# Performance work log

Measured on AMD Instinct MI355X. Metric: run time of the kernel, lower is better.

The kernel has to match this reference:

```python
import jax, jax.numpy as jnp
import numpy as np

DM = 1024; NHEAD = 16; HD = 64; ROPE = 32; KVC = 256; QC = 384
NSEQ = 4; SPS = 256; S = NSEQ * SPS + 1; B = 2
SCALE = 1.0 / ((HD + ROPE) // 2)          # 1/48, per module
LAMBDA_INIT = 0.8 - 0.6 * float(np.exp(-0.3 * 0))  # depth=0 -> 0.2
EPS_RMS = 1.1920929e-07                   # torch default RMSNorm eps (finfo eps)
EPS_HEAD = 1e-5


def _make_freqs(sps):
    # precompute_freqs_cis with args.seq_len=SPS, qk_rope_dim=ROPE (YaRN correction)
    dim = ROPE // 2
    base = 10000.0
    factor = 40.0
    seq_len = SPS
    max_seqlen = seq_len * 4
    freqs = 1.0 / base ** (np.arange(0, dim, 2, dtype=np.float32) / dim)  # (dim//2,)

    def corr_dim(nr):
        return dim * np.log(seq_len / (nr * 2 * np.pi)) / (2 * np.log(base))

    low = max(int(np.floor(corr_dim(32.0))), 0)
    high = min(int(np.ceil(corr_dim(1.0))), dim - 1)
    if low == high:
        high = high + 0.001
    ramp = np.clip((np.arange(dim // 2, dtype=np.float32) - low) / (high - low), 0, 1)
    smooth = 1.0 - ramp
    freqs = freqs / factor * (1 - smooth) + freqs * smooth
    t = np.arange(max_seqlen, dtype=np.float32)
    ang = np.outer(t, freqs)  # (max_seqlen, dim//2)
    return np.cos(ang)[:sps].astype(np.float32), np.sin(ang)[:sps].astype(np.float32)


def _make_mask():
    # global-separator mask: column 0 attendable, rest = tiled causal-per-timestep blocks
    temp = np.triu(np.ones((SPS, SPS), dtype=np.int32), k=1)
    tiled = np.tile(temp, (NSEQ, NSEQ))
    full = np.ones((S, S), dtype=np.int32)
    full[:, 0] = 0
    full[1:, 1:] = tiled
    return full[None, None]  # (1,1,S,S), 1 = masked


def _rms(x, g, eps):
    return x * jax.lax.rsqrt(jnp.mean(x * x, axis=-1, keepdims=True) + eps) * g


def _rope(x, cos, sin):
    # x: (b, nseq, sps, 2*nhead, ROPE//2) -> rotate complex pairs in last dim
    b, ns, sps, h, d = x.shape
    xr = x.reshape(b, ns, sps, h, d // 2, 2)
    c = cos[None, None, :, None, :]
    s = sin[None, None, :, None, :]
    yr = xr[..., 0] * c - xr[..., 1] * s
    yi = xr[..., 0] * s + xr[..., 1] * c
    return jnp.stack([yr, yi], axis=-1).reshape(b, ns, sps, h, d)


def setup_inputs() -> dict:
    key = jax.random.key(0)
    ks = jax.random.split(key, 12)
    cos, sin = _make_freqs(SPS)
    inp = {
        "x": jax.random.normal(ks[0], (B, S, DM), dtype=jnp.float32),
        "mask": jnp.asarray(_make_mask()),
        "freqs_cos": jnp.asarray(cos),
        "freqs_sin": jnp.asarray(sin),
        "W_kv_down": jax.random.normal(ks[1], (DM, KVC + ROPE), dtype=jnp.float32) * 0.02,
        "W_q_down": jax.random.normal(ks[2], (DM, QC), dtype=jnp.float32) * 0.02,
        "W_kv_up": jax.random.normal(ks[3], (KVC, NHEAD * HD * 2), dtype=jnp.float32) * 0.02,
        "W_q_up": jax.random.normal(ks[4], (QC, NHEAD * (HD + ROPE)), dtype=jnp.float32) * 0.02,
        "W_o": jax.random.normal(ks[5], (NHEAD * HD, DM), dtype=jnp.float32) * 0.02,
        "g_kv_norm": jnp.ones((KVC,), dtype=jnp.float32),
        "g_q_norm": jnp.ones((QC,), dtype=jnp.float32),
        "g_head_norm": jnp.ones((HD,), dtype=jnp.float32),
        "lambda_q1": jax.random.normal(ks[6], (HD // 2,), dtype=jnp.float32) * 0.1,
        "lambda_k1": jax.random.normal(ks[7], (HD // 2,), dtype=jnp.float32) * 0.1,
        "lambda_q2": jax.random.normal(ks[8], (HD // 2,), dtype=jnp.float32) * 0.1,
        "lambda_k2": jax.random.normal(ks[9], (HD // 2,), dtype=jnp.float32) * 0.1,
    }
    return inp


def reference(x, mask, freqs_cos, freqs_sin, W_kv_down, W_q_down, W_kv_up, W_q_up,
              W_o, g_kv_norm, g_q_norm, g_head_norm,
              lambda_q1, lambda_k1, lambda_q2, lambda_k2):
    b, s, _ = x.shape
    sps = (s - 1) // NSEQ
    # KV latent compression
    ckv = x @ W_kv_down                                   # (b,S,KVC+ROPE)
    c_kv, k_rope = ckv[..., :KVC], ckv[..., KVC:]
    kv = _rms(c_kv, g_kv_norm, EPS_RMS) @ W_kv_up         # (b,S,NHEAD*2*HD)
    kv = kv.reshape(b, s, NHEAD, 2 * HD)
    k, v = kv[..., :HD], kv[..., HD:]
    k = k.reshape(b, s, NHEAD * 2, HD // 2)               # dual head-groups
    # Q latent compression
    qf = _rms(x @ W_q_down, g_q_norm, EPS_RMS) @ W_q_up
    qf = qf.reshape(b, s, NHEAD, HD + ROPE)
    q, q_rope = qf[..., :HD], qf[..., HD:]
    q = q.reshape(b, s, NHEAD * 2, HD // 2)
    # RoPE parts: shared k_rope tiled over heads, then split into dual groups
    k_rope = jnp.tile(k_rope[:, :, None, :], (1, 1, NHEAD, 1)).reshape(b, s, NHEAD * 2, ROPE // 2)
    q_rope = q_rope.reshape(b, s, NHEAD * 2, ROPE // 2)
    # rotate all positions except the global separator token (index 0)
    q_rot = _rope(q_rope[:, 1:].reshape(b, NSEQ, sps, NHEAD * 2, ROPE // 2), freqs_cos, freqs_sin)
    k_rot = _rope(k_rope[:, 1:].reshape(b, NSEQ, sps, NHEAD * 2, ROPE // 2), freqs_cos, freqs_sin)
    q_rope = jnp.concatenate([q_rope[:, :1], q_rot.reshape(b, s - 1, NHEAD * 2, ROPE // 2)], axis=1)
    k_rope = jnp.concatenate([k_rope[:, :1], k_rot.reshape(b, s - 1, NHEAD * 2, ROPE // 2)], axis=1)
    q = jnp.concatenate([q, q_rope], axis=-1).transpose(0, 2, 1, 3)  # (b,2H,S,48)
    k = jnp.concatenate([k, k_rope], axis=-1).transpose(0, 2, 1, 3)
    v = v.transpose(0, 2, 1, 3)                                      # (b,H,S,64)
    # cognitive (signed) softmax attention
    a = jnp.einsum('bhqd,bhkd->bhqk', q, k) * SCALE
    abs_a = jnp.where(mask == 1, -1e9, jnp.abs(a))
    a = jnp.sign(a) * jax.nn.softmax(abs_a, axis=-1)
    # differential combination of dual head-groups
    lam = (jnp.exp(jnp.sum(lambda_q1 * lambda_k1)) -
           jnp.exp(jnp.sum(lambda_q2 * lambda_k2)) + LAMBDA_INIT)
    a = a.reshape(b, NHEAD, 2, s, s)
    G = jnp.mean(a[:, :, 0], axis=-1, keepdims=True)
    a = a[:, :, 0] - lam * a[:, :, 1] + G * lam
    a = jnp.where(mask == 1, 0.0, a)
    out = jnp.einsum('bhqk,bhkd->bhqd', a, v).transpose(0, 2, 1, 3)  # (b,S,H,64)
    out = _rms(out, g_head_norm, EPS_HEAD)
    return out.reshape(b, s, NHEAD * HD) @ W_o
```

## Files before the change

### kernel.cpp

```cpp
#include <hip/hip_runtime.h>
#include <hip/hip_bf16.h>
#include <math.h>

#define NHEAD 16
#define SEQ 1025
#define BATCH 2
#define NH2 32
#define KSCALE (1.0f/48.0f)
#define EPS_RMS 1.1920929e-07f
#define EPS_HEAD 1e-05f
#define LAMBDA_INIT 0.2f
#define R_TOT (BATCH*SEQ)

typedef __attribute__((ext_vector_type(8))) short bf16x8;
typedef __attribute__((ext_vector_type(4))) float f32x4;
typedef __attribute__((ext_vector_type(4))) int  i32x4;

static __device__ __forceinline__ unsigned short f2bf(float x) {
    unsigned int u = __float_as_uint(x);
    unsigned int r = (u + 0x7fffu + ((u >> 16) & 1u)) >> 16;
    return (unsigned short)r;
}
static __device__ __forceinline__ float bf2f(unsigned short h) {
    return __uint_as_float(((unsigned int)h) << 16);
}
static __device__ __forceinline__ void split3(float v, unsigned short& h,
                                              unsigned short& m, unsigned short& l) {
    h = f2bf(v); float r1 = v - bf2f(h);
    m = f2bf(r1); float r2 = r1 - bf2f(m);
    l = f2bf(r2);
}
static __device__ __forceinline__ f32x4 MFMA(bf16x8 a, bf16x8 b, f32x4 c) {
    return __builtin_amdgcn_mfma_f32_16x16x32_bf16(a, b, c, 0, 0, 0);
}

__global__ __launch_bounds__(256) void conv_all(
    const float* __restrict__ x, const float* __restrict__ Wkvd,
    const float* __restrict__ Wqd, const float* __restrict__ Wkvu,
    const float* __restrict__ Wqu, const float* __restrict__ Wo,
    unsigned short* __restrict__ xh, unsigned short* __restrict__ xm,
    unsigned short* __restrict__ xl,
    unsigned short* __restrict__ Wdh, unsigned short* __restrict__ Wdm,
    unsigned short* __restrict__ Wdl,
    unsigned short* __restrict__ Wuh, unsigned short* __restrict__ Wum,
    unsigned short* __restrict__ Wul,
    unsigned short* __restrict__ Wqh, unsigned short* __restrict__ Wqm,
    unsigned short* __restrict__ Wql,
    unsigned short* __restrict__ Wo1)
{
    __shared__ float tile[32][33];
    int bid = blockIdx.x, tid = threadIdx.x;
    if (bid < 2050) {
        int i = bid * 1024 + tid * 4;
        f32x4 v = *(const f32x4*)(x + i);
#pragma unroll
        for (int j = 0; j < 4; ++j) {
            unsigned short h, m, l;
            split3(v[j], h, m, l);
            xh[i + j] = h; xm[i + j] = m; xl[i + j] = l;
        }
        return;
    }
    bid -= 2050;
    const float* W; unsigned short *Th, *Tm, *Tl; int K, N, gx;
    if (bid < 288)              { W = Wkvd; Th = Wdh; Tm = Wdm; Tl = Wdl; K = 1024; N = 288;  gx = 9;  }
    else if ((bid -= 288) < 384){ W = Wqd;  Th = Wdh + (size_t)288*1024; Tm = Wdm + (size_t)288*1024;
                                  Tl = Wdl + (size_t)288*1024; K = 1024; N = 384; gx = 12; }
    else if ((bid -= 384) < 512){ W = Wkvu; Th = Wuh; Tm = Wum; Tl = Wul; K = 256;  N = 2048; gx = 64; }
    else if ((bid -= 512) < 576){ W = Wqu;  Th = Wqh; Tm = Wqm; Tl = Wql; K = 384;  N = 1536; gx = 48; }
    else { bid -= 576;            W = Wo;   Th = Wo1; Tm = nullptr; Tl = nullptr; K = 1024; N = 1024; gx = 32; }

    int n0 = (bid % gx) * 32, k0 = (bid / gx) * 32;
    int tx = tid & 31, ty = tid >> 5;
    for (int kk = ty; kk < 32; kk += 8)
        tile[kk][tx] = W[(size_t)(k0 + kk) * N + n0 + tx];
    __syncthreads();
    for (int nn = ty; nn < 32; nn += 8) {
        int n = n0 + nn, k = k0 + tx;
        float v = tile[tx][nn];
        if (Tm) {
            unsigned short h, m, l;
            split3(v, h, m, l);
            Th[(size_t)n * K + k] = h;
            Tm[(size_t)n * K + k] = m;
            Tl[(size_t)n * K + k] = l;
        } else {
            Th[(size_t)n * K + k] = f2bf(v);
        }
    }
}

__device__ __forceinline__ void gemm3_body(
    unsigned short* LA, unsigned short* LB,
    const unsigned short* __restrict__ Ah, const unsigned short* __restrict__ Am,
    const unsigned short* __restrict__ Al,
    const unsigned short* __restrict__ Bh, const unsigned short* __restrict__ Bm,
    const unsigned short* __restrict__ Bl,
    float* __restrict__ C,
    unsigned short* __restrict__ D0, unsigned short* __restrict__ D1,
    unsigned short* __restrict__ D2, unsigned short* __restrict__ D3,
    const float* __restrict__ fcos, const float* __restrict__ fsin,
    int M, int N, int K, int kb, int ke, int epi, int bm, int bn)
{
    int tid = threadIdx.x;
    int wid = tid >> 6, lane = tid & 63;
    int la = lane & 15, lb = lane >> 4;
    int wr = (wid >> 1) * 64, wc = (wid & 1) * 64;
    int wr4 = wr >> 4, wc4 = wc >> 4;

    const unsigned short* APl[3] = {Ah, Am, Al};
    const unsigned short* BPl[3] = {Bh, Bm, Bl};

    f32x4 acc[4][4];
#pragma unroll
    for (int m = 0; m < 4; ++m)
#pragma unroll
        for (int n = 0; n < 4; ++n) acc[m][n] = (f32x4){0.f, 0.f, 0.f, 0.f};

    auto LDF = [&](bf16x8* dst, const unsigned short* Lb, int p, int rb) {
#pragma unroll
        for (int q = 0; q < 4; ++q)
            dst[q] = *(const bf16x8*)&Lb[p * 4096 + ((rb + q) * 64 + lane) * 8];
    };
    auto MM = [&](bf16x8* av, bf16x8* bv) {
#pragma unroll
        for (int m = 0; m < 4; ++m)
#pragma unroll
            for (int n = 0; n < 4; ++n)
                acc[m][n] = MFMA(av[m], bv[n], acc[m][n]);
    };

    for (int k0 = kb; k0 < ke; k0 += 32) {
        __syncthreads();
#pragma unroll
        for (int p = 0; p < 3; ++p) {
#pragma unroll
            for (int it = 0; it < 2; ++it) {
                int k2 = tid + it * 256;
                int g = k2 >> 6, pos = k2 & 63;
                int row = (g << 4) + (pos & 15);
                int kc = (pos >> 4) * 8;
                i32x4 v = {0, 0, 0, 0}, w = {0, 0, 0, 0};
                int gr = bm + row;
                if (gr < M) v = *(const i32x4*)(APl[p] + (size_t)gr * K + k0 + kc);
                *(i32x4*)&LA[p * 4096 + k2 * 8] = v;
                int gn = bn + row;
                if (gn < N) w = *(const i32x4*)(BPl[p] + (size_t)gn * K + k0 + kc);
                *(i32x4*)&LB[p * 4096 + k2 * 8] = w;
            }
        }
        __syncthreads();
        bf16x8 av[4], bv0[4], bv1[4], bvt[4];
        LDF(av, LA, 0, wr4); LDF(bv0, LB, 0, wc4);
        LDF(bv1, LB, 1, wc4); LDF(bvt, LB, 2, wc4);
        __builtin_amdgcn_s_setprio(1);
        MM(av, bv0); MM(av, bv1); MM(av, bvt);
        __builtin_amdgcn_s_setprio(0);
        LDF(bvt, LA, 1, wr4);
        __builtin_amdgcn_s_setprio(1);
        MM(bvt, bv0); MM(bvt, bv1);
        __builtin_amdgcn_s_setprio(0);
        LDF(bvt, LA, 2, wr4);
        __builtin_amdgcn_s_setprio(1);
        MM(bvt, bv0);
        __builtin_amdgcn_s_setprio(0);
    }

#pragma unroll
    for (int m = 0; m < 4; ++m)
#pragma unroll
        for (int n = 0; n < 4; ++n) {
            int gc = bn + wc + n * 16 + la;
#pragma unroll
            for (int r = 0; r < 4; ++r) {
                int gr = bm + wr + m * 16 + lb * 4 + r;
                float v = acc[m][n][r];
                if (epi == 0) {
                    if (gr < M && gc < N) C[(size_t)gr * N + gc] = v;
                } else if (epi == 1) {
                    if (gr < M) {
                        int b = gr / SEQ, s = gr - b * SEQ;
                        int h2 = gc >> 7, rem = gc & 127;
                        if (rem < 64) {
                            int H = 2 * h2 + (rem >> 5), d = rem & 31;
                            size_t idx = (((size_t)b * NH2 + H) * SEQ + s) * 48 + d;
                            unsigned short hh, mm2, ll;
                            split3(v, hh, mm2, ll);
                            D0[idx] = hh; D1[idx] = mm2; D2[idx] = ll;
                        } else {
                            D3[(((size_t)b * NHEAD + h2) * SEQ + s) * 64 + (rem - 64)] = f2bf(v);
                        }
                    }
                } else {
                    float pv = __shfl_xor(v, 1);
                    if (gr < M) {
                        int b = gr / SEQ, s = gr - b * SEQ;
                        int h2 = gc / 96, rem = gc - h2 * 96;
                        int H, d; float outv;
                        if (rem < 64) {
                            H = 2 * h2 + (rem >> 5); d = rem & 31; outv = v;
                        } else {
                            int dd = rem - 64;
                            int e = dd >> 4, j = (dd & 15) >> 1;
                            H = 2 * h2 + e; d = 32 + (dd & 15);
                            if (s != 0) {
                                int p = (s - 1) & 255;
                                float cc = fcos[p * 8 + j], sn = fsin[p * 8 + j];
                                outv = ((la & 1) == 0) ? (v * cc - pv * sn)
                                                       : (pv * sn + v * cc);
                            } else outv = v;
                        }
                        outv *= KSCALE;
                        size_t idx = (((size_t)b * NH2 + H) * SEQ + s) * 48 + d;
                        unsigned short hh, mm2, ll;
                        split3(outv, hh, mm2, ll);
                        D0[idx] = hh; D1[idx] = mm2; D2[idx] = ll;
                    }
                }
            }
        }
}

__global__ __launch_bounds__(256) void gemm_down(
    const unsigned short* __restrict__ Ah, const unsigned short* __restrict__ Am,
    const unsigned short* __restrict__ Al,
    const unsigned short* __restrict__ Bh, const unsigned short* __restrict__ Bm,
    const unsigned short* __restrict__ Bl,
    float* __restrict__ C0, float* __restrict__ C1)
{
    __shared__ __align__(16) unsigned short LA[3 * 4096];
    __shared__ __align__(16) unsigned short LB[3 * 4096];
    int z = blockIdx.z;
    gemm3_body(LA, LB, Ah, Am, Al, Bh, Bm, Bl, z ? C1 : C0,
               nullptr, nullptr, nullptr, nullptr, nullptr, nullptr,
               R_TOT, 672, 1024, z * 512, z * 512 + 512, 0,
               blockIdx.y * 128, blockIdx.x * 128);
}

__global__ __launch_bounds__(256) void gemm_up(
    const unsigned short* __restrict__ cnh, const unsigned short* __restrict__ cnm,
    const unsigned short* __restrict__ cnl,
    const unsigned short* __restrict__ Wuh, const unsigned short* __restrict__ Wum,
    const unsigned short* __restrict__ Wul,
    const unsigned short* __restrict__ qnh, const unsigned short* __restrict__ qnm,
    const unsigned short* __restrict__ qnl,
    const unsigned short* __restrict__ Wqh, const unsigned short* __restrict__ Wqm,
    const unsigned short* __restrict__ Wql,
    unsigned short* __restrict__ Kah, unsigned short* __restrict__ Kam,
    unsigned short* __restrict__ Kal, unsigned short* __restrict__ Va,
    unsigned short* __restrict__ Qah, unsigned short* __restrict__ Qam,
    unsigned short* __restrict__ Qal,
    const float* __restrict__ fcos, const float* __restrict__ fsin)
{
    __shared__ __align__(16) unsigned short LA[3 * 4096];
    __shared__ __align__(16) unsigned short LB[3 * 4096];
    bool isq = (blockIdx.x >= 16);
    if (!isq)
        gemm3_body(LA, LB, cnh, cnm, cnl, Wuh, Wum, Wul, nullptr,
                   Kah, Kam, Kal, Va, nullptr, nullptr,
                   R_TOT, 2048, 256, 0, 256, 1, blockIdx.y * 128, blockIdx.x * 128);
    else
        gemm3_body(LA, LB, qnh, qnm, qnl, Wqh, Wqm, Wql, nullptr,
                   Qah, Qam, Qal, nullptr, fcos, fsin,
                   R_TOT, 1536, 384, 0, 384, 2, blockIdx.y * 128, (blockIdx.x - 16) * 128);
}

__global__ __launch_bounds__(256) void gemm_out(
    const unsigned short* __restrict__ Ah, const unsigned short* __restrict__ Bh,
    float* __restrict__ C, int M, int N, int K)
{
    __shared__ __align__(16) unsigned short As[4096];
    __shared__ __align__(16) unsigned short Bs[4096];
    int tid = threadIdx.x;
    int wid = tid >> 6, lane = tid & 63;
    int la = lane & 15, lb = lane >> 4;
    int bm = blockIdx.y * 128, bn = blockIdx.x * 128;
    int wr = (wid >> 1) * 64, wc = (wid & 1) * 64;
    int wr4 = wr >> 4, wc4 = wc >> 4;
    f32x4 acc[4][4];
#pragma unroll
    for (int m = 0; m < 4; ++m)
#pragma unroll
        for (int n = 0; n < 4; ++n) acc[m][n] = (f32x4){0.f, 0.f, 0.f, 0.f};
    for (int k0 = 0; k0 < K; k0 += 32) {
        __syncthreads();
#pragma unroll
        for (int it = 0; it < 2; ++it) {
            int k2 = tid + it * 256;
            int g = k2 >> 6, pos = k2 & 63;
            int row = (g << 4) + (pos & 15);
            int kc = (pos >> 4) * 8;
            i32x4 v = {0, 0, 0, 0}, w = {0, 0, 0, 0};
            int gr = bm + row;
            if (gr < M) v = *(const i32x4*)(Ah + (size_t)gr * K + k0 + kc);
            *(i32x4*)&As[k2 * 8] = v;
            int gn = bn + row;
            if (gn < N) w = *(const i32x4*)(Bh + (size_t)gn * K + k0 + kc);
            *(i32x4*)&Bs[k2 * 8] = w;
        }
        __syncthreads();
        bf16x8 a_[4], b_[4];
#pragma unroll
        for (int m = 0; m < 4; ++m) a_[m] = *(const bf16x8*)&As[((wr4 + m) * 64 + lane) * 8];
#pragma unroll
        for (int n = 0; n < 4; ++n) b_[n] = *(const bf16x8*)&Bs[((wc4 + n) * 64 + lane) * 8];
        __builtin_amdgcn_s_setprio(1);
#pragma unroll
        for (int m = 0; m < 4; ++m)
#pragma unroll
            for (int n = 0; n < 4; ++n) acc[m][n] = MFMA(a_[m], b_[n], acc[m][n]);
        __builtin_amdgcn_s_setprio(0);
    }
#pragma unroll
    for (int m = 0; m < 4; ++m)
#pragma unroll
        for (int n = 0; n < 4; ++n) {
            int gc = bn + wc + n * 16 + la;
            if (gc >= N) continue;
#pragma unroll
            for (int r = 0; r < 4; ++r) {
                int gr = bm + wr + m * 16 + lb * 4 + r;
                if (gr < M) C[(size_t)gr * N + gc] = acc[m][n][r];
            }
        }
}

__global__ __launch_bounds__(256) void k_rmsrope3(
    const float* __restrict__ ckvqd, const float* __restrict__ ckvqd2,
    unsigned short* __restrict__ cnh, unsigned short* __restrict__ cnm,
    unsigned short* __restrict__ cnl,
    unsigned short* __restrict__ qnh, unsigned short* __restrict__ qnm,
    unsigned short* __restrict__ qnl,
    unsigned short* __restrict__ Kah, unsigned short* __restrict__ Kam,
    unsigned short* __restrict__ Kal,
    const float* __restrict__ gkv, const float* __restrict__ gq,
    const float* __restrict__ fcos, const float* __restrict__ fsin)
{
    __shared__ float red[256];
    __shared__ float rot[32];
    int row = blockIdx.x, tid = threadIdx.x;
    int b = row / SEQ, s = row - b * SEQ;
    const float* cp  = ckvqd  + (size_t)row * 672;
    const float* cp2 = ckvqd2 + (size_t)row * 672;
    float c0 = cp[tid] + cp2[tid];
    float q0 = cp[288 + tid] + cp2[288 + tid];
    float q1 = (tid < 128) ? (cp[544 + tid] + cp2[544 + tid]) : 0.f;

    red[tid] = c0 * c0;
    __syncthreads();
    for (int o = 128; o; o >>= 1) { if (tid < o) red[tid] += red[tid + o]; __syncthreads(); }
    float inv1 = rsqrtf(red[0] * (1.f / 256.f) + EPS_RMS);
    __syncthreads();
    red[tid] = q0 * q0 + q1 * q1;
    __syncthreads();
    for (int o = 128; o; o >>= 1) { if (tid < o) red[tid] += red[tid + o]; __syncthreads(); }
    float inv2 = rsqrtf(red[0] * (1.f / 384.f) + EPS_RMS);

    unsigned short h, m, l;
    split3(c0 * inv1 * gkv[tid], h, m, l);
    size_t ci = (size_t)row * 256 + tid;
    cnh[ci] = h; cnm[ci] = m; cnl[ci] = l;

    split3(q0 * inv2 * gq[tid], h, m, l);
    size_t qi = (size_t)row * 384 + tid;
    qnh[qi] = h; qnm[qi] = m; qnl[qi] = l;
    if (tid < 128) {
        split3(q1 * inv2 * gq[256 + tid], h, m, l);
        qnh[qi + 256] = h; qnm[qi + 256] = m; qnl[qi + 256] = l;
    }

    if (tid < 16) {
        float r0 = cp[256 + 2 * tid] + cp2[256 + 2 * tid];
        float r1 = cp[256 + 2 * tid + 1] + cp2[256 + 2 * tid + 1];
        float o0, o1;
        if (s == 0) { o0 = r0; o1 = r1; }
        else {
            int p = (s - 1) & 255;
            int j = tid & 7;
            float cc = fcos[p * 8 + j], sn = fsin[p * 8 + j];
            o0 = r0 * cc - r1 * sn;
            o1 = r0 * sn + r1 * cc;
        }
        rot[2 * tid] = o0; rot[2 * tid + 1] = o1;
    }
    __syncthreads();
    for (int t = tid; t < 512; t += 256) {
        int H = t >> 4, dd = t & 15;
        int e = H & 1;
        split3(rot[e * 16 + dd], h, m, l);
        size_t idx = (((size_t)b * NH2 + H) * SEQ + s) * 48 + 32 + dd;
        Kah[idx] = h; Kam[idx] = m; Kal[idx] = l;
    }
}

__global__ __launch_bounds__(256, 2) void k_attn8(
    const unsigned short* __restrict__ Qah, const unsigned short* __restrict__ Qam,
    const unsigned short* __restrict__ Qal,
    const unsigned short* __restrict__ Kah, const unsigned short* __restrict__ Kam,
    const unsigned short* __restrict__ Kal,
    const unsigned short* __restrict__ Va, const float* __restrict__ ghead,
    const float* __restrict__ lq1, const float* __restrict__ lk1,
    const float* __restrict__ lq2, const float* __restrict__ lk2,
    unsigned short* __restrict__ attO)
{
    __shared__ __align__(16) unsigned short KS[6][3072];
    __shared__ __align__(16) unsigned short Vt[4096];
    __shared__ __align__(16) unsigned short Pl[4][1024];

    int bid0 = blockIdx.x;
    int bid = (bid0 & 7) * 68 + (bid0 >> 3);
    int rt = bid % 17;
    int bh = bid / 17;
    int h = bh & 15, b = bh >> 4;
    int tid = threadIdx.x, wid = tid >> 6, lane = tid & 63;
    int la = lane & 15, lb = lane >> 4;
    int r0 = rt * 64, r0w = r0 + wid * 16;

    float e1 = 0.f, e2 = 0.f;
    for (int i = 0; i < 32; ++i) { e1 = fmaf(lq1[i], lk1[i], e1); e2 = fmaf(lq2[i], lk2[i], e2); }
    float lam = __expf(e1) - __expf(e2) + LAMBDA_INIT;

    int pr[4];
#pragma unroll
    for (int g = 0; g < 4; ++g) {
        int r = r0w + lb * 4 + g;
        pr[g] = (r >= 1 && r < SEQ) ? ((r - 1) & 255) : -1;
    }
    int rA = r0w + la;
    int prA = (rA >= 1 && rA < SEQ) ? ((rA - 1) & 255) : -1;

    int prm = -1;
    for (int i = 0; i < 64; ++i) {
        int r = r0 + i;
        if (r >= 1 && r < SEQ) { int p = (r - 1) & 255; prm = p > prm ? p : prm; }
    }

    const size_t hb1 = ((size_t)(b * NH2 + 2 * h)) * SEQ * 48;
    const size_t hb2 = ((size_t)(b * NH2 + 2 * h + 1)) * SEQ * 48;
    const unsigned short* vp = Va + ((size_t)(b * NHEAD + h)) * SEQ * 64;
    const unsigned short* KP[6] = {Kah + hb1, Kam + hb1, Kal + hb1,
                                   Kah + hb2, Kam + hb2, Kal + hb2};

    int qrow = r0w + la; if (qrow > SEQ - 1) qrow = SEQ - 1;
    bf16x8 zf;
#pragma unroll
    for (int u = 0; u < 8; ++u) zf[u] = 0;
    bf16x8 q1[3][2], q2[3][2];
    {
        const unsigned short* QPl[3] = {Qah, Qam, Qal};
#pragma unroll
        for (int p = 0; p < 3; ++p)
#pragma unroll
            for (int f = 0; f < 2; ++f) {
                if (f == 0 || lb < 2) {
                    q1[p][f] = *(const bf16x8*)(QPl[p] + hb1 + (size_t)qrow * 48 + 32 * f + lb * 8);
                    q2[p][f] = *(const bf16x8*)(QPl[p] + hb2 + (size_t)qrow * 48 + 32 * f + lb * 8);
                } else { q1[p][f] = zf; q2[p][f] = zf; }
            }
    }

    int colA, uA, colB = 0, uB = 0;
    {
        int ci = tid;
        colA = ((ci >> 6) << 4) + (ci & 15);
        uA = (ci >> 4) & 3;
        if (tid < 128) {
            int c2 = tid;
            colB = ((c2 >> 5) << 4) + (c2 & 15);
            uB = 4 + ((c2 >> 4) & 1);
        }
    }
    int cv0 = tid >> 3, uv0 = tid & 7;
    int cv1 = (tid + 256) >> 3, uv1 = tid & 7;

    i32x4 preA[6], preB[6], vv[2];
    auto LOADT = [&](int c0n) {
        int gcA = c0n + colA; if (gcA > SEQ - 1) gcA = SEQ - 1;
#pragma unroll
        for (int p = 0; p < 6; ++p)
            preA[p] = *(const i32x4*)(KP[p] + (size_t)gcA * 48 + uA * 8);
        if (tid < 128) {
            int gcB = c0n + colB; if (gcB > SEQ - 1) gcB = SEQ - 1;
#pragma unroll
            for (int p = 0; p < 6; ++p)
                preB[p] = *(const i32x4*)(KP[p] + (size_t)gcB * 48 + uB * 8);
        }
        int gv0 = c0n + cv0; if (gv0 > SEQ - 1) gv0 = SEQ - 1;
        vv[0] = *(const i32x4*)(vp + (size_t)gv0 * 64 + uv0 * 8);
        int gv1 = c0n + cv1; if (gv1 > SEQ - 1) gv1 = SEQ - 1;
        vv[1] = *(const i32x4*)(vp + (size_t)gv1 * 64 + uv1 * 8);
    };
    auto WRITET = [&]() {
#pragma unroll
        for (int p = 0; p < 6; ++p)
            *(i32x4*)&KS[p][tid * 8] = preA[p];
        if (tid < 128) {
#pragma unroll
            for (int p = 0; p < 6; ++p)
                *(i32x4*)&KS[p][2048 + tid * 8] = preB[p];
        }
#pragma unroll
        for (int it = 0; it < 2; ++it) {
            int cv = it ? cv1 : cv0, uv = it ? uv1 : uv0;
            unsigned short tmp[8];
            *(i32x4*)tmp = vv[it];
#pragma unroll
            for (int j = 0; j < 8; ++j) {
                int d = uv * 8 + j;
                int g = ((d >> 4) << 1) + (cv >> 5);
                int pos = (((cv & 31) >> 3) << 4) + (d & 15);
                Vt[g * 512 + pos * 8 + (cv & 7)] = tmp[j];
            }
        }
    };

    f32x4 O1[4], O2[4], VS[4];
#pragma unroll
    for (int nd = 0; nd < 4; ++nd) {
        O1[nd] = (f32x4){0.f, 0.f, 0.f, 0.f};
        O2[nd] = (f32x4){0.f, 0.f, 0.f, 0.f};
        VS[nd] = (f32x4){0.f, 0.f, 0.f, 0.f};
    }
    float dA1[4] = {0.f, 0.f, 0.f, 0.f}, dA2[4] = {0.f, 0.f, 0.f, 0.f};
    float gsA[4] = {0.f, 0.f, 0.f, 0.f};
    f32x4 z = (f32x4){0.f, 0.f, 0.f, 0.f};

    LOADT(0);
    WRITET();
    __syncthreads();

    for (int j = 0; j <= 16; ++j) {
        bool need = (j == 16) ? (prm >= 255)
                              : (((j & 3) == 0) || (prm >= 64 * (j & 3) - 1));
        if (!need) continue;
        int c0 = j * 64;

        int nj = -1;
        for (int t2 = j + 1; t2 <= 16; ++t2) {
            bool nd2 = (t2 == 16) ? (prm >= 255)
                                  : (((t2 & 3) == 0) || (prm >= 64 * (t2 & 3) - 1));
            if (nd2) { nj = t2; break; }
        }
        if (nj >= 0) LOADT(nj * 64);

        f32x4 s1[4], s2[4];
        __builtin_amdgcn_s_setprio(1);
#pragma unroll
        for (int n = 0; n < 4; ++n) {
            int g0 = n * 512 + lane * 8;
            int g1 = 2048 + n * 256 + (lane & 31) * 8;
            bf16x8 kh0 = *(const bf16x8*)&KS[0][g0];
            bf16x8 kh1 = *(const bf16x8*)&KS[0][g1];
            bf16x8 km0 = *(const bf16x8*)&KS[1][g0];
            bf16x8 km1 = *(const bf16x8*)&KS[1][g1];
            bf16x8 kl0 = *(const bf16x8*)&KS[2][g0];
            bf16x8 kl1 = *(const bf16x8*)&KS[2][g1];
            f32x4 s = z;
            s = MFMA(q1[0][0], kh0, s); s = MFMA(q1[0][1], kh1, s);
            s = MFMA(q1[0][0], km0, s); s = MFMA(q1[0][1], km1, s);
            s = MFMA(q1[1][0], kh0, s); s = MFMA(q1[1][1], kh1, s);
            s = MFMA(q1[0][0], kl0, s); s = MFMA(q1[0][1], kl1, s);
            s = MFMA(q1[1][0], km0, s); s = MFMA(q1[1][1], km1, s);
            s = MFMA(q1[2][0], kh0, s); s = MFMA(q1[2][1], kh1, s);
            s1[n] = s;
        }
#pragma unroll
        for (int n = 0; n < 4; ++n) {
            int g0 = n * 512 + lane * 8;
            int g1 = 2048 + n * 256 + (lane & 31) * 8;
            bf16x8 kh0 = *(const bf16x8*)&KS[3][g0];
            bf16x8 kh1 = *(const bf16x8*)&KS[3][g1];
            bf16x8 km0 = *(const bf16x8*)&KS[4][g0];
            bf16x8 km1 = *(const bf16x8*)&KS[4][g1];
            bf16x8 kl0 = *(const bf16x8*)&KS[5][g0];
            bf16x8 kl1 = *(const bf16x8*)&KS[5][g1];
            f32x4 s = z;
            s = MFMA(q2[0][0], kh0, s); s = MFMA(q2[0][1], kh1, s);
            s = MFMA(q2[0][0], km0, s); s = MFMA(q2[0][1], km1, s);
            s = MFMA(q2[1][0], kh0, s); s = MFMA(q2[1][1], kh1, s);
            s = MFMA(q2[0][0], kl0, s); s = MFMA(q2[0][1], kl1, s);
            s = MFMA(q2[1][0], km0, s); s = MFMA(q2[1][1], km1, s);
            s = MFMA(q2[2][0], kh0, s); s = MFMA(q2[2][1], kh1, s);
            s2[n] = s;
        }
        __builtin_amdgcn_s_setprio(0);

        unsigned short p1v[4][4], p2v[4][4];
#pragma unroll
        for (int n = 0; n < 4; ++n) {
            int c = c0 + n * 16 + la;
            bool cz = (c == 0);
            int cm = (c - 1) & 255;
            bool cin = (c < SEQ);
#pragma unroll
            for (int g = 0; g < 4; ++g) {
                bool al = cz || (cin && cm <= pr[g]);
                float a = s1[n][g];
                float sa = __builtin_copysignf(__expf(fabsf(a)), a);
                sa = al ? sa : 0.f;
                p1v[n][g] = (unsigned short)((__float_as_uint(sa) + 0x8000u) >> 16);
                gsA[g] += sa;
                dA1[g] += fabsf(sa);
                float bb = s2[n][g];
                float sb = __builtin_copysignf(__expf(fabsf(bb)), bb);
                sb = al ? sb : 0.f;
                p2v[n][g] = (unsigned short)((__float_as_uint(sb) + 0x8000u) >> 16);
                dA2[g] += fabsf(sb);
            }
        }

#pragma unroll
        for (int n = 0; n < 4; ++n) {
            int pb = (n >> 1) * 512 + (((n & 1) << 1) + (la >> 3)) * 128 + (la & 7);
#pragma unroll
            for (int g = 0; g < 4; ++g)
                Pl[wid][pb + (lb * 4 + g) * 8] = p1v[n][g];
        }
        __asm__ volatile("s_waitcnt lgkmcnt(0)" ::: "memory");
        __builtin_amdgcn_sched_barrier(0);
        bf16x8 p1a0 = *(const bf16x8*)&Pl[wid][lane * 8];
        bf16x8 p1a1 = *(const bf16x8*)&Pl[wid][512 + lane * 8];
#pragma unroll
        for (int n = 0; n < 4; ++n) {
            int pb = (n >> 1) * 512 + (((n & 1) << 1) + (la >> 3)) * 128 + (la & 7);
#pragma unroll
            for (int g = 0; g < 4; ++g)
                Pl[wid][pb + (lb * 4 + g) * 8] = p2v[n][g];
        }
        __asm__ volatile("s_waitcnt lgkmcnt(0)" ::: "memory");
        __builtin_amdgcn_sched_barrier(0);
        bf16x8 p2a0 = *(const bf16x8*)&Pl[wid][lane * 8];
        bf16x8 p2a1 = *(const bf16x8*)&Pl[wid][512 + lane * 8];

        bf16x8 p0[2];
#pragma unroll
        for (int f = 0; f < 2; ++f)
#pragma unroll
            for (int jb = 0; jb < 8; ++jb) {
                int c = c0 + 32 * f + lb * 8 + jb;
                bool al = (c == 0) || (c < SEQ && ((c - 1) & 255) <= prA);
                p0[f][jb] = al ? (short)0x3F80 : (short)0;
            }

        __builtin_amdgcn_s_setprio(1);
#pragma unroll
        for (int nd = 0; nd < 4; ++nd) {
            bf16x8 vb0 = *(const bf16x8*)&Vt[(nd * 2) * 512 + lane * 8];
            bf16x8 vb1 = *(const bf16x8*)&Vt[(nd * 2 + 1) * 512 + lane * 8];
            O1[nd] = MFMA(p1a0, vb0, O1[nd]);
            O1[nd] = MFMA(p1a1, vb1, O1[nd]);
            O2[nd] = MFMA(p2a0, vb0, O2[nd]);
            O2[nd] = MFMA(p2a1, vb1, O2[nd]);
            VS[nd] = MFMA(p0[0], vb0, VS[nd]);
            VS[nd] = MFMA(p0[1], vb1, VS[nd]);
        }
        __builtin_amdgcn_s_setprio(0);

        if (nj >= 0) {
            __syncthreads();
            WRITET();
            __syncthreads();
        }
    }

#pragma unroll
    for (int off = 1; off < 16; off <<= 1) {
#pragma unroll
        for (int g = 0; g < 4; ++g) {
            dA1[g] += __shfl_xor(dA1[g], off);
            dA2[g] += __shfl_xor(dA2[g], off);
            gsA[g] += __shfl_xor(gsA[g], off);
        }
    }

    float i1[4], i2g[4], Gl[4];
#pragma unroll
    for (int g = 0; g < 4; ++g) {
        i1[g] = 1.f / dA1[g];
        i2g[g] = 1.f / dA2[g];
        Gl[g] = gsA[g] * i1[g] * (1.f / (float)SEQ) * lam;
    }
    f32x4 outv[4];
#pragma unroll
    for (int nd = 0; nd < 4; ++nd)
#pragma unroll
        for (int g = 0; g < 4; ++g)
            outv[nd][g] = O1[nd][g] * i1[g] - lam * i2g[g] * O2[nd][g] + Gl[g] * VS[nd][g];

    float ssq[4] = {0.f, 0.f, 0.f, 0.f};
#pragma unroll
    for (int nd = 0; nd < 4; ++nd)
#pragma unroll
        for (int g = 0; g < 4; ++g) ssq[g] += outv[nd][g] * outv[nd][g];
#pragma unroll
    for (int off = 1; off < 16; off <<= 1)
#pragma unroll
        for (int g = 0; g < 4; ++g) ssq[g] += __shfl_xor(ssq[g], off);
    float inv[4];
#pragma unroll
    for (int g = 0; g < 4; ++g) inv[g] = rsqrtf(ssq[g] * (1.f / 64.f) + EPS_HEAD);

#pragma unroll
    for (int nd = 0; nd < 4; ++nd) {
        int d = nd * 16 + la;
        float gv = ghead[d];
#pragma unroll
        for (int g = 0; g < 4; ++g) {
            int r = r0w + lb * 4 + g;
            if (r < SEQ)
                attO[(((size_t)b * SEQ + r) * NHEAD + h) * 64 + d] =
                    f2bf(outv[nd][g] * inv[g] * gv);
        }
    }
}

extern "C" void kernel_launch(void* const* d_in, const int* in_sizes, int n_in,
                              void* d_out, int out_size, void* d_ws, size_t ws_size,
                              hipStream_t stream)
{
    const float* x    = (const float*)d_in[0];
    const float* fcos = (const float*)d_in[2];
    const float* fsin = (const float*)d_in[3];
    const float* Wkvd = (const float*)d_in[4];
    const float* Wqd  = (const float*)d_in[5];
    const float* Wkvu = (const float*)d_in[6];
    const float* Wqu  = (const float*)d_in[7];
    const float* Wo   = (const float*)d_in[8];
    const float* gkv  = (const float*)d_in[9];
    const float* gq   = (const float*)d_in[10];
    const float* gh   = (const float*)d_in[11];
    const float* lq1  = (const float*)d_in[12];
    const float* lk1  = (const float*)d_in[13];
    const float* lq2  = (const float*)d_in[14];
    const float* lk2  = (const float*)d_in[15];
    float* out = (float*)d_out;

    const int R = R_TOT;
    char* base = (char*)d_ws;
    size_t off = 0;
    auto alloc = [&](size_t bytes) -> char* {
        char* p = base + off;
        off = (off + bytes + 255) & ~(size_t)255;
        return p;
    };
    const size_t KPL = (size_t)BATCH * NH2 * SEQ * 48 * 2;

    unsigned short* xh = (unsigned short*)alloc((size_t)R * 1024 * 2);
    unsigned short* xm = (unsigned short*)alloc((size_t)R * 1024 * 2);
    unsigned short* xl = (unsigned short*)alloc((size_t)R * 1024 * 2);
    unsigned short* attO = xh;
    unsigned short* Kah  = xm;

    float* ckvqd = (float*)alloc((size_t)R * 672 * 4);
    unsigned short* cnh = (unsigned short*)alloc((size_t)R * 256 * 2);
    unsigned short* cnm = (unsigned short*)alloc((size_t)R * 256 * 2);
    unsigned short* cnl = (unsigned short*)alloc((size_t)R * 256 * 2);
    unsigned short* qnh = (unsigned short*)alloc((size_t)R * 384 * 2);
    unsigned short* qnm = (unsigned short*)alloc((size_t)R * 384 * 2);
    unsigned short* qnl = (unsigned short*)alloc((size_t)R * 384 * 2);
    unsigned short* Kam = (unsigned short*)alloc(KPL);
    unsigned short* Kal = (unsigned short*)alloc(KPL);
    unsigned short* Qah = (unsigned short*)alloc(KPL);
    unsigned short* Qam = (unsigned short*)alloc(KPL);
    unsigned short* Qal = (unsigned short*)alloc(KPL);
    unsigned short* Va  = (unsigned short*)alloc((size_t)BATCH * NHEAD * SEQ * 64 * 2);
    unsigned short* Wdh = (unsigned short*)alloc((size_t)672 * 1024 * 2);
    unsigned short* Wdm = (unsigned short*)alloc((size_t)672 * 1024 * 2);
    unsigned short* Wdl = (unsigned short*)alloc((size_t)672 * 1024 * 2);
    unsigned short* Wuh = (unsigned short*)alloc((size_t)2048 * 256 * 2);
    unsigned short* Wum = (unsigned short*)alloc((size_t)2048 * 256 * 2);
    unsigned short* Wul = (unsigned short*)alloc((size_t)2048 * 256 * 2);
    unsigned short* Wqh = (unsigned short*)alloc((size_t)1536 * 384 * 2);
    unsigned short* Wqm = (unsigned short*)alloc((size_t)1536 * 384 * 2);
    unsigned short* Wql = (unsigned short*)alloc((size_t)1536 * 384 * 2);
    unsigned short* Wo1 = (unsigned short*)alloc((size_t)1024 * 1024 * 2);

    float* ckvqd2 = (float*)Qah;

    dim3 blk(256);
    conv_all<<<4834, blk, 0, stream>>>(x, Wkvd, Wqd, Wkvu, Wqu, Wo,
        xh, xm, xl, Wdh, Wdm, Wdl, Wuh, Wum, Wul, Wqh, Wqm, Wql, Wo1);
    gemm_down<<<dim3(6, 17, 2), blk, 0, stream>>>(xh, xm, xl, Wdh, Wdm, Wdl,
                                                  ckvqd, ckvqd2);
    k_rmsrope3<<<R, blk, 0, stream>>>(ckvqd, ckvqd2, cnh, cnm, cnl, qnh, qnm, qnl,
                                      Kah, Kam, Kal, gkv, gq, fcos, fsin);
    gemm_up<<<dim3(28, 17), blk, 0, stream>>>(cnh, cnm, cnl, Wuh, Wum, Wul,
        qnh, qnm, qnl, Wqh, Wqm, Wql, Kah, Kam, Kal, Va, Qah, Qam, Qal, fcos, fsin);
    k_attn8<<<544, blk, 0, stream>>>(Qah, Qam, Qal, Kah, Kam, Kal,
        Va, gh, lq1, lk1, lq2, lk2, attO);
    gemm_out<<<dim3(8, 17), blk, 0, stream>>>(attO, Wo1, out, R, 1024, 1024);
}
```

Before: 317.4 us.

## Split attention key loop across two blocks and reduce partials in separate kernel

The attention kernel now launches twice as many blocks, and each one processes alternating key tiles, like a split-K over the key dimension. Partial unnormalized O1/O2 (fp32), VS (bf16) and the row sums are written to workspace buffers. A new reduction kernel adds the two halves, applies the lambda differential combination and the head RMSNorm, and writes attO. The aim is more parallelism and better CU occupancy for a grid of 544 blocks, at the cost of extra global traffic, an extra launch, and rounding VS partials to bf16.

```diff
diff --git a/kernel.cpp b/kernel.cpp
--- a/kernel.cpp
+++ b/kernel.cpp
@@ -11,6 +11,8 @@
 #define EPS_HEAD 1e-05f
 #define LAMBDA_INIT 0.2f
 #define R_TOT (BATCH*SEQ)
+#define NL 544
+#define NROWS (NL*64)
 
 typedef __attribute__((ext_vector_type(8))) short bf16x8;
 typedef __attribute__((ext_vector_type(4))) float f32x4;
@@ -393,32 +395,36 @@
     }
 }
 
-__global__ __launch_bounds__(256, 2) void k_attn8(
+__global__ __launch_bounds__(256, 2) void k_attn9(
     const unsigned short* __restrict__ Qah, const unsigned short* __restrict__ Qam,
     const unsigned short* __restrict__ Qal,
     const unsigned short* __restrict__ Kah, const unsigned short* __restrict__ Kam,
     const unsigned short* __restrict__ Kal,
-    const unsigned short* __restrict__ Va, const float* __restrict__ ghead,
-    const float* __restrict__ lq1, const float* __restrict__ lk1,
-    const float* __restrict__ lq2, const float* __restrict__ lk2,
-    unsigned short* __restrict__ attO)
+    const unsigned short* __restrict__ Va,
+    float* __restrict__ PO1a, float* __restrict__ PO1b,
+    float* __restrict__ PO2a, float* __restrict__ PO2b,
+    unsigned short* __restrict__ PVSa, unsigned short* __restrict__ PVSb,
+    float* __restrict__ psa, float* __restrict__ psb)
 {
     __shared__ __align__(16) unsigned short KS[6][3072];
     __shared__ __align__(16) unsigned short Vt[4096];
     __shared__ __align__(16) unsigned short Pl[4][1024];
 
     int bid0 = blockIdx.x;
-    int bid = (bid0 & 7) * 68 + (bid0 >> 3);
-    int rt = bid % 17;
-    int bh = bid / 17;
+    int half = bid0 & 1;
+    int pid0 = bid0 >> 1;
+    int L = (pid0 & 7) * 68 + (pid0 >> 3);
+    int rt = L % 17;
+    int bh = L / 17;
     int h = bh & 15, b = bh >> 4;
     int tid = threadIdx.x, wid = tid >> 6, lane = tid & 63;
     int la = lane & 15, lb = lane >> 4;
     int r0 = rt * 64, r0w = r0 + wid * 16;
 
-    float e1 = 0.f, e2 = 0.f;
-    for (int i = 0; i < 32; ++i) { e1 = fmaf(lq1[i], lk1[i], e1); e2 = fmaf(lq2[i], lk2[i], e2); }
-    float lam = __expf(e1) - __expf(e2) + LAMBDA_INIT;
+    float* PO1 = half ? PO1b : PO1a;
+    float* PO2 = half ? PO2b : PO2a;
+    unsigned short* PVS = half ? PVSb : PVSa;
+    float* ps = half ? psb : psa;
 
     int pr[4];
 #pragma unroll
@@ -434,6 +440,10 @@
         int r = r0 + i;
         if (r >= 1 && r < SEQ) { int p = (r - 1) & 255; prm = p > prm ? p : prm; }
     }
+    auto needf = [&](int t) -> bool {
+        return (t == 16) ? (prm >= 255)
+                         : (((t & 3) == 0) || (prm >= 64 * (t & 3) - 1));
+    };
 
     const size_t hb1 = ((size_t)(b * NH2 + 2 * h)) * SEQ * 48;
     const size_t hb2 = ((size_t)(b * NH2 + 2 * h + 1)) * SEQ * 48;
@@ -525,21 +535,23 @@
     float gsA[4] = {0.f, 0.f, 0.f, 0.f};
     f32x4 z = (f32x4){0.f, 0.f, 0.f, 0.f};
 
-    LOADT(0);
+    int fj = 0;
+    {
+        int c2 = 0;
+        for (int j = 0; j <= 16; ++j)
+            if (needf(j)) { if (c2 == half) { fj = j; break; } c2++; }
+    }
+    LOADT(fj * 64);
     WRITET();
     __syncthreads();
 
-    for (int j = 0; j <= 16; ++j) {
-        bool need = (j == 16) ? (prm >= 255)
-                              : (((j & 3) == 0) || (prm >= 64 * (j & 3) - 1));
-        if (!need) continue;
+    for (int j = fj; j <= 16;) {
         int c0 = j * 64;
-
-        int nj = -1;
+        int nj = -1, skip = 0;
         for (int t2 = j + 1; t2 <= 16; ++t2) {
-            bool nd2 = (t2 == 16) ? (prm >= 255)
-                                  : (((t2 & 3) == 0) || (prm >= 64 * (t2 & 3) - 1));
-            if (nd2) { nj = t2; break; }
+            if (!needf(t2)) continue;
+            if (skip) { nj = t2; break; }
+            skip = 1;
         }
         if (nj >= 0) LOADT(nj * 64);
 
@@ -656,11 +668,11 @@
         }
         __builtin_amdgcn_s_setprio(0);
 
-        if (nj >= 0) {
-            __syncthreads();
-            WRITET();
-            __syncthreads();
-        }
+        if (nj < 0) break;
+        __syncthreads();
+        WRITET();
+        __syncthreads();
+        j = nj;
     }
 
 #pragma unroll
@@ -673,43 +685,78 @@
         }
     }
 
-    float i1[4], i2g[4], Gl[4];
-#pragma unroll
-    for (int g = 0; g < 4; ++g) {
-        i1[g] = 1.f / dA1[g];
-        i2g[g] = 1.f / dA2[g];
-        Gl[g] = gsA[g] * i1[g] * (1.f / (float)SEQ) * lam;
-    }
-    f32x4 outv[4];
-#pragma unroll
-    for (int nd = 0; nd < 4; ++nd)
-#pragma unroll
-        for (int g = 0; g < 4; ++g)
-            outv[nd][g] = O1[nd][g] * i1[g] - lam * i2g[g] * O2[nd][g] + Gl[g] * VS[nd][g];
-
-    float ssq[4] = {0.f, 0.f, 0.f, 0.f};
-#pragma unroll
-    for (int nd = 0; nd < 4; ++nd)
-#pragma unroll
-        for (int g = 0; g < 4; ++g) ssq[g] += outv[nd][g] * outv[nd][g];
-#pragma unroll
-    for (int off = 1; off < 16; off <<= 1)
-#pragma unroll
-        for (int g = 0; g < 4; ++g) ssq[g] += __shfl_xor(ssq[g], off);
-    float inv[4];
-#pragma unroll
-    for (int g = 0; g < 4; ++g) inv[g] = rsqrtf(ssq[g] * (1.f / 64.f) + EPS_HEAD);
-
+    size_t rb = (size_t)L * 64 + wid * 16 + lb * 4;
+    if (la == 0) {
+#pragma unroll
+        for (int g = 0; g < 4; ++g) {
+            ps[rb + g] = dA1[g];
+            ps[NROWS + rb + g] = dA2[g];
+            ps[2 * NROWS + rb + g] = gsA[g];
+        }
+    }
 #pragma unroll
     for (int nd = 0; nd < 4; ++nd) {
         int d = nd * 16 + la;
-        float gv = ghead[d];
 #pragma unroll
         for (int g = 0; g < 4; ++g) {
-            int r = r0w + lb * 4 + g;
-            if (r < SEQ)
-                attO[(((size_t)b * SEQ + r) * NHEAD + h) * 64 + d] =
-                    f2bf(outv[nd][g] * inv[g] * gv);
+            size_t idx = (rb + g) * 64 + d;
+            PO1[idx] = O1[nd][g];
+            PO2[idx] = O2[nd][g];
+            PVS[idx] = f2bf(VS[nd][g]);
+        }
+    }
+}
+
+__global__ __launch_bounds__(256) void k_ared(
+    const float* __restrict__ PO1a, const float* __restrict__ PO1b,
+    const float* __restrict__ PO2a, const float* __restrict__ PO2b,
+    const unsigned short* __restrict__ PVSa, const unsigned short* __restrict__ PVSb,
+    const float* __restrict__ psa, const float* __restrict__ psb,
+    const float* __restrict__ ghead,
+    const float* __restrict__ lq1, const float* __restrict__ lk1,
+    const float* __restrict__ lq2, const float* __restrict__ lk2,
+    unsigned short* __restrict__ attO)
+{
+    int L = blockIdx.x;
+    int rt = L % 17, bh = L / 17;
+    int h = bh & 15, b = bh >> 4;
+    int tid = threadIdx.x;
+    int r = tid >> 2, q = tid & 3;
+
+    float e1 = 0.f, e2 = 0.f;
+    for (int i = 0; i < 32; ++i) { e1 = fmaf(lq1[i], lk1[i], e1); e2 = fmaf(lq2[i], lk2[i], e2); }
+    float lam = __expf(e1) - __expf(e2) + LAMBDA_INIT;
+
+    size_t rb = (size_t)L * 64 + r;
+    float d1 = psa[rb] + psb[rb];
+    float d2 = psa[NROWS + rb] + psb[NROWS + rb];
+    float gs = psa[2 * NROWS + rb] + psb[2 * NROWS + rb];
+    float i1 = 1.f / d1, i2 = 1.f / d2;
+    float Gl = gs * i1 * (1.f / (float)SEQ) * lam;
+
+    float outv[16];
+    float ssq = 0.f;
+    size_t ob = rb * 64 + q * 16;
+#pragma unroll
+    for (int k = 0; k < 16; ++k) {
+        float o1 = PO1a[ob + k] + PO1b[ob + k];
+        float o2 = PO2a[ob + k] + PO2b[ob + k];
+        float vs = bf2f(PVSa[ob + k]) + bf2f(PVSb[ob + k]);
+        float v = o1 * i1 - lam * i2 * o2 + Gl * vs;
+        outv[k] = v;
+        ssq += v * v;
+    }
+    ssq += __shfl_xor(ssq, 1);
+    ssq += __shfl_xor(ssq, 2);
+    float inv = rsqrtf(ssq * (1.f / 64.f) + EPS_HEAD);
+
+    int rw = rt * 64 + r;
+    if (rw < SEQ) {
+#pragma unroll
+        for (int k = 0; k < 16; ++k) {
+            int d = q * 16 + k;
+            attO[(((size_t)b * SEQ + rw) * NHEAD + h) * 64 + d] =
+                f2bf(outv[k] * inv * ghead[d]);
         }
     }
 }
@@ -777,6 +824,18 @@
 
     float* ckvqd2 = (float*)Qah;
 
+    const size_t POB = (size_t)NROWS * 64 * 4;
+    const size_t PVB = (size_t)NROWS * 64 * 2;
+    const size_t PSB = (size_t)3 * NROWS * 4;
+    float* PO1a = (float*)ckvqd;
+    unsigned short* PVSa = (unsigned short*)((char*)ckvqd + POB);
+    float* PO1b = (float*)Wdh;
+    float* PO2a = (float*)alloc(POB);
+    float* PO2b = (float*)alloc(POB);
+    unsigned short* PVSb = (unsigned short*)alloc(PVB);
+    float* psa = (float*)alloc(PSB);
+    float* psb = (float*)alloc(PSB);
+
     dim3 blk(256);
     conv_all<<<4834, blk, 0, stream>>>(x, Wkvd, Wqd, Wkvu, Wqu, Wo,
         xh, xm, xl, Wdh, Wdm, Wdl, Wuh, Wum, Wul, Wqh, Wqm, Wql, Wo1);
@@ -786,7 +845,9 @@
                                       Kah, Kam, Kal, gkv, gq, fcos, fsin);
     gemm_up<<<dim3(28, 17), blk, 0, stream>>>(cnh, cnm, cnl, Wuh, Wum, Wul,
         qnh, qnm, qnl, Wqh, Wqm, Wql, Kah, Kam, Kal, Va, Qah, Qam, Qal, fcos, fsin);
-    k_attn8<<<544, blk, 0, stream>>>(Qah, Qam, Qal, Kah, Kam, Kal,
-        Va, gh, lq1, lk1, lq2, lk2, attO);
+    k_attn9<<<1088, blk, 0, stream>>>(Qah, Qam, Qal, Kah, Kam, Kal, Va,
+        PO1a, PO1b, PO2a, PO2b, PVSa, PVSb, psa, psb);
+    k_ared<<<NL, blk, 0, stream>>>(PO1a, PO1b, PO2a, PO2b, PVSa, PVSb,
+        psa, psb, gh, lq1, lk1, lq2, lk2, attO);
     gemm_out<<<dim3(8, 17), blk, 0, stream>>>(attO, Wo1, out, R, 1024, 1024);
 }
```

After: 332.6 us. 4.8% more time.
